# Kernel tuning notes

Measured on AMD Instinct MI355X. Metric: run time of the kernel, lower is better.

The kernel has to match this reference:

```python
import jax, jax.numpy as jnp
import numpy as np

B, S, D, H, W = 8, 2048, 128, 8, 64
INT_HEADS = 8          # hardcoded in SpatioTemporalLayer1
EPS_COS = 1e-8
EPS_LN = 1e-5


def _mha(q_in, k_in, v_in, in_w, in_b, out_w, out_b, nh, mask=None):
    # q_in/k_in/v_in: (batch, len, d); torch nn.MultiheadAttention math (eval, no dropout)
    b, lq, d = q_in.shape
    hd = d // nh
    q = (q_in @ in_w[:d].T + in_b[:d]).reshape(b, lq, nh, hd)
    k = (k_in @ in_w[d:2 * d].T + in_b[d:2 * d]).reshape(b, k_in.shape[1], nh, hd)
    v = (v_in @ in_w[2 * d:].T + in_b[2 * d:]).reshape(b, v_in.shape[1], nh, hd)
    scores = jnp.einsum('bihd,bjhd->bhij', q, k) / jnp.sqrt(jnp.asarray(hd, q_in.dtype))
    if mask is not None:
        scores = scores + mask
    attn = jax.nn.softmax(scores, axis=-1)
    out = jnp.einsum('bhij,bjhd->bihd', attn, v).reshape(b, lq, d)
    return out @ out_w.T + out_b


def _layernorm(x, g, b):
    mu = x.mean(-1, keepdims=True)
    var = ((x - mu) ** 2).mean(-1, keepdims=True)
    return (x - mu) * jax.lax.rsqrt(var + EPS_LN) * g + b


def _cos_normalize(e):
    n = jnp.maximum(jnp.linalg.norm(e, axis=-1, keepdims=True), EPS_COS)
    return e / n


def _forward(x, spatial_info, temporal_info,
             lw_in_w, lw_in_b, lw_out_w, lw_out_b,
             spat_w, spat_b, temp_w, temp_b,
             int_in_w, int_in_b, int_out_w, int_out_b,
             ffn_w1, ffn_b1, ffn_w2, ffn_b2,
             ln1_g, ln1_b, ln2_g, ln2_b):
    b, s, d = x.shape
    # --- local window attention (S % W == 0 here, so no padding path) ---
    nw = s // W
    xw = x.reshape(b * nw, W, d)
    causal = jnp.triu(jnp.full((W, W), -jnp.inf, x.dtype), k=1)
    attn = _mha(xw, xw, xw, lw_in_w, lw_in_b, lw_out_w, lw_out_b, H, causal).reshape(b, s, d)
    x = _layernorm(attn + x, ln1_g, ln1_b)
    # --- FFN (torch nn.GELU default = exact erf) ---
    h = jax.nn.gelu(x @ ffn_w1.T + ffn_b1, approximate=False)
    x = _layernorm(h @ ffn_w2.T + ffn_b2 + x, ln2_g, ln2_b)
    # --- spatio-temporal interaction ---
    se = spatial_info @ spat_w.T + spat_b
    te = temporal_info @ temp_w.T + temp_b
    sn = _cos_normalize(se)
    tn = _cos_normalize(te)
    ss = jnp.einsum('bid,bjd->bij', sn, sn)   # (B,S,S) spatial cosine sim
    ts = jnp.einsum('bid,bjd->bij', tn, tn)   # (B,S,S) temporal cosine sim
    # interaction MHA is batch_first=False: it treats (B,S,D) as (len=B, batch=S, d).
    # Equivalent batch-first call on swapped axes (faithful to the torch source).
    inter = jnp.swapaxes(
        _mha(jnp.swapaxes(se, 0, 1), jnp.swapaxes(te, 0, 1), jnp.swapaxes(te, 0, 1),
             int_in_w, int_in_b, int_out_w, int_out_b, INT_HEADS), 0, 1)
    # similarity[b,i,j,d] = ss[b,i,j]*ts[b,i,j]*inter[b,i,d]; mean over j factorizes:
    sim = (ss * ts).mean(axis=2)              # (B,S)
    return x + sim[..., None] * inter


def setup_inputs() -> dict:
    key = jax.random.key(0)
    ks = jax.random.split(key, 24)
    sc = 0.02
    inp = {
        'x': jax.random.normal(ks[0], (B, S, D), jnp.float32),
        'spatial_info': jax.random.normal(ks[1], (B, S, D), jnp.float32),
        'temporal_info': jax.random.normal(ks[2], (B, S, D), jnp.float32),
        'lw_in_w': jax.random.normal(ks[3], (3 * D, D), jnp.float32) * sc,
        'lw_in_b': jnp.zeros((3 * D,), jnp.float32),
        'lw_out_w': jax.random.normal(ks[4], (D, D), jnp.float32) * sc,
        'lw_out_b': jnp.zeros((D,), jnp.float32),
        'spat_w': jax.random.normal(ks[5], (D, D), jnp.float32) * sc,
        'spat_b': jnp.zeros((D,), jnp.float32),
        'temp_w': jax.random.normal(ks[6], (D, D), jnp.float32) * sc,
        'temp_b': jnp.zeros((D,), jnp.float32),
        'int_in_w': jax.random.normal(ks[7], (3 * D, D), jnp.float32) * sc,
        'int_in_b': jnp.zeros((3 * D,), jnp.float32),
        'int_out_w': jax.random.normal(ks[8], (D, D), jnp.float32) * sc,
        'int_out_b': jnp.zeros((D,), jnp.float32),
        'ffn_w1': jax.random.normal(ks[9], (4 * D, D), jnp.float32) * sc,
        'ffn_b1': jnp.zeros((4 * D,), jnp.float32),
        'ffn_w2': jax.random.normal(ks[10], (D, 4 * D), jnp.float32) * sc,
        'ffn_b2': jnp.zeros((D,), jnp.float32),
        'ln1_g': jnp.ones((D,), jnp.float32),
        'ln1_b': jnp.zeros((D,), jnp.float32),
        'ln2_g': jnp.ones((D,), jnp.float32),
        'ln2_b': jnp.zeros((D,), jnp.float32),
    }
    return inp


def reference(x, spatial_info, temporal_info,
              lw_in_w, lw_in_b, lw_out_w, lw_out_b,
              spat_w, spat_b, temp_w, temp_b,
              int_in_w, int_in_b, int_out_w, int_out_b,
              ffn_w1, ffn_b1, ffn_w2, ffn_b2,
              ln1_g, ln1_b, ln2_g, ln2_b):
    return _forward(x, spatial_info, temporal_info,
                    lw_in_w, lw_in_b, lw_out_w, lw_out_b,
                    spat_w, spat_b, temp_w, temp_b,
                    int_in_w, int_in_b, int_out_w, int_out_b,
                    ffn_w1, ffn_b1, ffn_w2, ffn_b2,
                    ln1_g, ln1_b, ln2_g, ln2_b)
```

## Files before the change

kernel.cpp:

```cpp
#include <hip/hip_runtime.h>
#include <math.h>

#define BB 8
#define SS 2048
#define NTOK (BB * SS)
#define ATB_SPLIT 16

using bf16x8 = __attribute__((ext_vector_type(8))) short;
using f32x4  = __attribute__((ext_vector_type(4))) float;

__device__ __forceinline__ float gelu_exact(float v) {
    return 0.5f * v * (1.0f + erff(v * 0.70710678118654752f));
}
__device__ __forceinline__ unsigned short f2b(float f) {
    unsigned int u = __float_as_uint(f);
    u += 0x7FFFu + ((u >> 16) & 1u);
    return (unsigned short)(u >> 16);
}
__device__ __forceinline__ float b2f(unsigned short u) {
    return __uint_as_float((unsigned int)u << 16);
}
__device__ __forceinline__ bf16x8 ldg_f32_b8(const float* p) {
    float4 f0 = *(const float4*)p, f1 = *(const float4*)(p + 4);
    union { ushort4 u[2]; bf16x8 v; } r;
    r.u[0] = (ushort4){f2b(f0.x), f2b(f0.y), f2b(f0.z), f2b(f0.w)};
    r.u[1] = (ushort4){f2b(f1.x), f2b(f1.y), f2b(f1.z), f2b(f1.w)};
    return r.v;
}

__global__ __launch_bounds__(256) void win_block(
    const float* __restrict__ x,
    const unsigned short* __restrict__ Wqkv,
    const float* __restrict__ b_in,
    const unsigned short* __restrict__ Wout,
    const float* __restrict__ b_out,
    const float* __restrict__ lng, const float* __restrict__ lnb,
    float* __restrict__ x1, unsigned short* __restrict__ x1b)
{
    __shared__ unsigned short Qs[64 * 136];
    __shared__ unsigned short KVs[64 * 256];
    __shared__ float red[2][64][2];
    const int tid = threadIdx.x, m0 = blockIdx.x * 64;
    const int wv = tid >> 6, lane = tid & 63, ln = lane & 15, q = lane >> 4;
    const int wm = (wv >> 1) * 32, wn = (wv & 1) * 64;

    bf16x8 afr[4][2];
    #pragma unroll
    for (int kf = 0; kf < 4; ++kf)
        #pragma unroll
        for (int fm = 0; fm < 2; ++fm)
            afr[kf][fm] = ldg_f32_b8(x + (size_t)(m0 + wm + fm * 16 + ln) * 128 + kf * 32 + q * 8);

    #pragma unroll
    for (int p = 0; p < 3; ++p) {
        f32x4 acc[2][4] = {};
        #pragma unroll
        for (int kf = 0; kf < 4; ++kf) {
            bf16x8 b[4];
            #pragma unroll
            for (int fn = 0; fn < 4; ++fn)
                b[fn] = *(const bf16x8*)&Wqkv[(size_t)(p * 128 + wn + fn * 16 + ln) * 128 + kf * 32 + q * 8];
            #pragma unroll
            for (int fm = 0; fm < 2; ++fm)
                #pragma unroll
                for (int fn = 0; fn < 4; ++fn)
                    acc[fm][fn] = __builtin_amdgcn_mfma_f32_16x16x32_bf16(afr[kf][fm], b[fn], acc[fm][fn], 0, 0, 0);
        }
        #pragma unroll
        for (int fm = 0; fm < 2; ++fm)
            #pragma unroll
            for (int r = 0; r < 4; ++r) {
                int rl = wm + fm * 16 + q * 4 + r;
                #pragma unroll
                for (int fn = 0; fn < 4; ++fn) {
                    int col = wn + fn * 16 + ln;
                    unsigned short v = f2b(acc[fm][fn][r] + b_in[p * 128 + col]);
                    if (p == 0) Qs[rl * 136 + col] = v;
                    else        KVs[rl * 256 + (p - 1) * 128 + col] = v;
                }
            }
    }
    __syncthreads();

    {
        const int l = tid & 63, hp = tid >> 6;
        #pragma unroll
        for (int hh = 0; hh < 2; ++hh) {
            const int h = hp + hh * 4;
            float qr[16];
            {
                uint4 q0 = *(const uint4*)&Qs[l * 136 + h * 16];
                uint4 q1 = *(const uint4*)&Qs[l * 136 + h * 16 + 8];
                const unsigned short* p0 = (const unsigned short*)&q0;
                const unsigned short* p1 = (const unsigned short*)&q1;
                #pragma unroll
                for (int c = 0; c < 8; ++c) { qr[c] = b2f(p0[c]); qr[8 + c] = b2f(p1[c]); }
            }
            float m = -1e30f, ssum = 0.0f, o[16] = {};
            for (int j = 0; j <= l; ++j) {
                uint4 k0 = *(const uint4*)&KVs[j * 256 + h * 16];
                uint4 k1 = *(const uint4*)&KVs[j * 256 + h * 16 + 8];
                const unsigned short* kp0 = (const unsigned short*)&k0;
                const unsigned short* kp1 = (const unsigned short*)&k1;
                float s = 0.0f;
                #pragma unroll
                for (int c = 0; c < 8; ++c) {
                    s = fmaf(qr[c], b2f(kp0[c]), s);
                    s = fmaf(qr[8 + c], b2f(kp1[c]), s);
                }
                s *= 0.25f;
                float mnew = fmaxf(m, s);
                float corr = expf(m - mnew);
                float pp = expf(s - mnew);
                ssum = ssum * corr + pp;
                uint4 v0 = *(const uint4*)&KVs[j * 256 + 128 + h * 16];
                uint4 v1 = *(const uint4*)&KVs[j * 256 + 128 + h * 16 + 8];
                const unsigned short* vp0 = (const unsigned short*)&v0;
                const unsigned short* vp1 = (const unsigned short*)&v1;
                #pragma unroll
                for (int c = 0; c < 8; ++c) {
                    o[c]     = o[c]     * corr + pp * b2f(vp0[c]);
                    o[8 + c] = o[8 + c] * corr + pp * b2f(vp1[c]);
                }
                m = mnew;
            }
            float inv = 1.0f / ssum;
            ushort4 w0, w1, w2, w3;
            w0 = (ushort4){f2b(o[0]*inv),  f2b(o[1]*inv),  f2b(o[2]*inv),  f2b(o[3]*inv)};
            w1 = (ushort4){f2b(o[4]*inv),  f2b(o[5]*inv),  f2b(o[6]*inv),  f2b(o[7]*inv)};
            w2 = (ushort4){f2b(o[8]*inv),  f2b(o[9]*inv),  f2b(o[10]*inv), f2b(o[11]*inv)};
            w3 = (ushort4){f2b(o[12]*inv), f2b(o[13]*inv), f2b(o[14]*inv), f2b(o[15]*inv)};
            *(ushort4*)&Qs[l * 136 + h * 16]      = w0;
            *(ushort4*)&Qs[l * 136 + h * 16 + 4]  = w1;
            *(ushort4*)&Qs[l * 136 + h * 16 + 8]  = w2;
            *(ushort4*)&Qs[l * 136 + h * 16 + 12] = w3;
        }
    }
    __syncthreads();

    f32x4 acc[2][4] = {};
    #pragma unroll
    for (int kf = 0; kf < 4; ++kf) {
        bf16x8 a[2], b[4];
        #pragma unroll
        for (int fm = 0; fm < 2; ++fm)
            a[fm] = *(const bf16x8*)&Qs[(wm + fm * 16 + ln) * 136 + kf * 32 + q * 8];
        #pragma unroll
        for (int fn = 0; fn < 4; ++fn)
            b[fn] = *(const bf16x8*)&Wout[(size_t)(wn + fn * 16 + ln) * 128 + kf * 32 + q * 8];
        #pragma unroll
        for (int fm = 0; fm < 2; ++fm)
            #pragma unroll
            for (int fn = 0; fn < 4; ++fn)
                acc[fm][fn] = __builtin_amdgcn_mfma_f32_16x16x32_bf16(a[fm], b[fn], acc[fm][fn], 0, 0, 0);
    }
    #pragma unroll
    for (int fm = 0; fm < 2; ++fm)
        #pragma unroll
        for (int r = 0; r < 4; ++r) {
            int rl = wm + fm * 16 + q * 4 + r;
            int row = m0 + rl;
            float s1 = 0.0f, s2 = 0.0f;
            #pragma unroll
            for (int fn = 0; fn < 4; ++fn) {
                int col = wn + fn * 16 + ln;
                float vv = acc[fm][fn][r] + b_out[col] + x[(size_t)row * 128 + col];
                acc[fm][fn][r] = vv;
                s1 += vv; s2 += vv * vv;
            }
            #pragma unroll
            for (int off = 1; off < 16; off <<= 1) {
                s1 += __shfl_xor(s1, off, 64);
                s2 += __shfl_xor(s2, off, 64);
            }
            if (ln == 0) { red[0][rl][wv & 1] = s1; red[1][rl][wv & 1] = s2; }
        }
    __syncthreads();
    #pragma unroll
    for (int fm = 0; fm < 2; ++fm)
        #pragma unroll
        for (int r = 0; r < 4; ++r) {
            int rl = wm + fm * 16 + q * 4 + r;
            int row = m0 + rl;
            float mu = (red[0][rl][0] + red[0][rl][1]) * (1.0f / 128.0f);
            float var = (red[1][rl][0] + red[1][rl][1]) * (1.0f / 128.0f) - mu * mu;
            float rs = rsqrtf(var + 1e-5f);
            #pragma unroll
            for (int fn = 0; fn < 4; ++fn) {
                int col = wn + fn * 16 + ln;
                float o = (acc[fm][fn][r] - mu) * rs * lng[col] + lnb[col];
                x1[(size_t)row * 128 + col] = o;
                x1b[(size_t)row * 128 + col] = f2b(o);
            }
        }
}

__global__ __launch_bounds__(256) void inter_block(
    const unsigned short* __restrict__ seb, const unsigned short* __restrict__ teb,
    const unsigned short* __restrict__ Wint,
    const float* __restrict__ b_int,
    const unsigned short* __restrict__ Wio,
    const float* __restrict__ b_io,
    const float* __restrict__ sim, const float* __restrict__ x2,
    float* __restrict__ out)
{
    __shared__ unsigned short Qs[64 * 136];
    __shared__ unsigned short KVs[64 * 256];
    const int tid = threadIdx.x, s0 = blockIdx.x * 8;
    const int wv = tid >> 6, lane = tid & 63, ln = lane & 15, q = lane >> 4;
    const int wm = (wv >> 1) * 32, wn = (wv & 1) * 64;

    bf16x8 afr[4][2];
    #pragma unroll
    for (int kf = 0; kf < 4; ++kf)
        #pragma unroll
        for (int fm = 0; fm < 2; ++fm) {
            int rl = wm + fm * 16 + ln;
            size_t g = (size_t)(rl >> 3) * 2048 + s0 + (rl & 7);
            afr[kf][fm] = *(const bf16x8*)&seb[g * 128 + kf * 32 + q * 8];
        }

    #pragma unroll
    for (int p = 0; p < 3; ++p) {
        if (p == 1) {
            #pragma unroll
            for (int kf = 0; kf < 4; ++kf)
                #pragma unroll
                for (int fm = 0; fm < 2; ++fm) {
                    int rl = wm + fm * 16 + ln;
                    size_t g = (size_t)(rl >> 3) * 2048 + s0 + (rl & 7);
                    afr[kf][fm] = *(const bf16x8*)&teb[g * 128 + kf * 32 + q * 8];
                }
        }
        f32x4 acc[2][4] = {};
        #pragma unroll
        for (int kf = 0; kf < 4; ++kf) {
            bf16x8 b[4];
            #pragma unroll
            for (int fn = 0; fn < 4; ++fn)
                b[fn] = *(const bf16x8*)&Wint[(size_t)(p * 128 + wn + fn * 16 + ln) * 128 + kf * 32 + q * 8];
            #pragma unroll
            for (int fm = 0; fm < 2; ++fm)
                #pragma unroll
                for (int fn = 0; fn < 4; ++fn)
                    acc[fm][fn] = __builtin_amdgcn_mfma_f32_16x16x32_bf16(afr[kf][fm], b[fn], acc[fm][fn], 0, 0, 0);
        }
        #pragma unroll
        for (int fm = 0; fm < 2; ++fm)
            #pragma unroll
            for (int r = 0; r < 4; ++r) {
                int rl = wm + fm * 16 + q * 4 + r;
                #pragma unroll
                for (int fn = 0; fn < 4; ++fn) {
                    int col = wn + fn * 16 + ln;
                    unsigned short v = f2b(acc[fm][fn][r] + b_int[p * 128 + col]);
                    if (p == 0) Qs[rl * 136 + col] = v;
                    else        KVs[rl * 256 + (p - 1) * 128 + col] = v;
                }
            }
        __syncthreads();
    }

    #pragma unroll
    for (int tt = 0; tt < 2; ++tt) {
        int task = tid + tt * 256;
        int ss = task >> 6, h = (task >> 3) & 7, i = task & 7;
        int rq = i * 8 + ss;
        float qr[16];
        {
            uint4 q0 = *(const uint4*)&Qs[rq * 136 + h * 16];
            uint4 q1 = *(const uint4*)&Qs[rq * 136 + h * 16 + 8];
            const unsigned short* p0 = (const unsigned short*)&q0;
            const unsigned short* p1 = (const unsigned short*)&q1;
            #pragma unroll
            for (int c = 0; c < 8; ++c) { qr[c] = b2f(p0[c]); qr[8 + c] = b2f(p1[c]); }
        }
        float sc[8];
        #pragma unroll
        for (int j = 0; j < 8; ++j) {
            uint4 k0 = *(const uint4*)&KVs[(j * 8 + ss) * 256 + h * 16];
            uint4 k1 = *(const uint4*)&KVs[(j * 8 + ss) * 256 + h * 16 + 8];
            const unsigned short* kp0 = (const unsigned short*)&k0;
            const unsigned short* kp1 = (const unsigned short*)&k1;
            float s = 0.0f;
            #pragma unroll
            for (int c = 0; c < 8; ++c) {
                s = fmaf(qr[c], b2f(kp0[c]), s);
                s = fmaf(qr[8 + c], b2f(kp1[c]), s);
            }
            sc[j] = s * 0.25f;
        }
        float mx = -1e30f;
        #pragma unroll
        for (int j = 0; j < 8; ++j) mx = fmaxf(mx, sc[j]);
        float pe[8], se = 0.0f;
        #pragma unroll
        for (int j = 0; j < 8; ++j) { pe[j] = expf(sc[j] - mx); se += pe[j]; }
        float inv = 1.0f / se;
        float o[16] = {};
        #pragma unroll
        for (int j = 0; j < 8; ++j) {
            uint4 v0 = *(const uint4*)&KVs[(j * 8 + ss) * 256 + 128 + h * 16];
            uint4 v1 = *(const uint4*)&KVs[(j * 8 + ss) * 256 + 128 + h * 16 + 8];
            const unsigned short* vp0 = (const unsigned short*)&v0;
            const unsigned short* vp1 = (const unsigned short*)&v1;
            #pragma unroll
            for (int c = 0; c < 8; ++c) {
                o[c]     += pe[j] * b2f(vp0[c]);
                o[8 + c] += pe[j] * b2f(vp1[c]);
            }
        }
        ushort4 w0 = (ushort4){f2b(o[0]*inv),  f2b(o[1]*inv),  f2b(o[2]*inv),  f2b(o[3]*inv)};
        ushort4 w1 = (ushort4){f2b(o[4]*inv),  f2b(o[5]*inv),  f2b(o[6]*inv),  f2b(o[7]*inv)};
        ushort4 w2 = (ushort4){f2b(o[8]*inv),  f2b(o[9]*inv),  f2b(o[10]*inv), f2b(o[11]*inv)};
        ushort4 w3 = (ushort4){f2b(o[12]*inv), f2b(o[13]*inv), f2b(o[14]*inv), f2b(o[15]*inv)};
        *(ushort4*)&Qs[rq * 136 + h * 16]      = w0;
        *(ushort4*)&Qs[rq * 136 + h * 16 + 4]  = w1;
        *(ushort4*)&Qs[rq * 136 + h * 16 + 8]  = w2;
        *(ushort4*)&Qs[rq * 136 + h * 16 + 12] = w3;
    }
    __syncthreads();

    f32x4 acc[2][4] = {};
    #pragma unroll
    for (int kf = 0; kf < 4; ++kf) {
        bf16x8 a[2], b[4];
        #pragma unroll
        for (int fm = 0; fm < 2; ++fm)
            a[fm] = *(const bf16x8*)&Qs[(wm + fm * 16 + ln) * 136 + kf * 32 + q * 8];
        #pragma unroll
        for (int fn = 0; fn < 4; ++fn)
            b[fn] = *(const bf16x8*)&Wio[(size_t)(wn + fn * 16 + ln) * 128 + kf * 32 + q * 8];
        #pragma unroll
        for (int fm = 0; fm < 2; ++fm)
            #pragma unroll
            for (int fn = 0; fn < 4; ++fn)
                acc[fm][fn] = __builtin_amdgcn_mfma_f32_16x16x32_bf16(a[fm], b[fn], acc[fm][fn], 0, 0, 0);
    }
    #pragma unroll
    for (int fm = 0; fm < 2; ++fm)
        #pragma unroll
        for (int r = 0; r < 4; ++r) {
            int rl = wm + fm * 16 + q * 4 + r;
            size_t g = (size_t)(rl >> 3) * 2048 + s0 + (rl & 7);
            float sc = sim[g];
            #pragma unroll
            for (int fn = 0; fn < 4; ++fn) {
                int col = wn + fn * 16 + ln;
                out[g * 128 + col] = (acc[fm][fn][r] + b_io[col]) * sc + x2[g * 128 + col];
            }
        }
}

__global__ __launch_bounds__(256) void ffn_fused(
    const unsigned short* __restrict__ x1b, const float* __restrict__ x1,
    const unsigned short* __restrict__ w1, const unsigned short* __restrict__ w2,
    const float* __restrict__ b1, const float* __restrict__ b2,
    const float* __restrict__ lng, const float* __restrict__ lnb,
    float* __restrict__ x2)
{
    __shared__ unsigned short Xs[64 * 136];
    __shared__ unsigned short Hs[64 * 72];
    __shared__ float red[2][64][2];
    const int tid = threadIdx.x, t0 = blockIdx.x * 64;
    const int wv = tid >> 6, lane = tid & 63, ln = lane & 15, q = lane >> 4;
    const int wm = (wv >> 1) * 32;
    const int wn1 = (wv & 1) * 32, wn2 = (wv & 1) * 64;

    const uint4* X4 = (const uint4*)(x1b + (size_t)t0 * 128);
    #pragma unroll
    for (int t = 0; t < 4; ++t) {
        int idx = tid + t * 256;
        int r = idx >> 4, c = idx & 15;
        *(uint4*)&Xs[r * 136 + c * 8] = X4[r * 16 + c];
    }
    __syncthreads();

    bf16x8 xfr[4][2];
    #pragma unroll
    for (int kf = 0; kf < 4; ++kf)
        #pragma unroll
        for (int fm = 0; fm < 2; ++fm)
            xfr[kf][fm] = *(const bf16x8*)&Xs[(wm + fm * 16 + ln) * 136 + kf * 32 + q * 8];

    f32x4 acc2[2][4] = {};
    for (int ch = 0; ch < 8; ++ch) {
        const int hc0 = ch * 64;
        f32x4 acc1[2][2] = {};
        #pragma unroll
        for (int kf = 0; kf < 4; ++kf) {
            bf16x8 b[2];
            #pragma unroll
            for (int fn = 0; fn < 2; ++fn)
                b[fn] = *(const bf16x8*)&w1[(size_t)(hc0 + wn1 + fn * 16 + ln) * 128 + kf * 32 + q * 8];
            #pragma unroll
            for (int fm = 0; fm < 2; ++fm)
                #pragma unroll
                for (int fn = 0; fn < 2; ++fn)
                    acc1[fm][fn] = __builtin_amdgcn_mfma_f32_16x16x32_bf16(xfr[kf][fm], b[fn], acc1[fm][fn], 0, 0, 0);
        }
        #pragma unroll
        for (int fm = 0; fm < 2; ++fm)
            #pragma unroll
            for (int fn = 0; fn < 2; ++fn)
                #pragma unroll
                for (int r = 0; r < 4; ++r) {
                    int rl = wm + fm * 16 + q * 4 + r;
                    int col = wn1 + fn * 16 + ln;
                    Hs[rl * 72 + col] = f2b(gelu_exact(acc1[fm][fn][r] + b1[hc0 + col]));
                }
        __syncthreads();
        #pragma unroll
        for (int kf = 0; kf < 2; ++kf) {
            bf16x8 a[2], b[4];
            #pragma unroll
            for (int fm = 0; fm < 2; ++fm)
                a[fm] = *(const bf16x8*)&Hs[(wm + fm * 16 + ln) * 72 + kf * 32 + q * 8];
            #pragma unroll
            for (int fn = 0; fn < 4; ++fn)
                b[fn] = *(const bf16x8*)&w2[(size_t)(wn2 + fn * 16 + ln) * 512 + hc0 + kf * 32 + q * 8];
            #pragma unroll
            for (int fm = 0; fm < 2; ++fm)
                #pragma unroll
                for (int fn = 0; fn < 4; ++fn)
                    acc2[fm][fn] = __builtin_amdgcn_mfma_f32_16x16x32_bf16(a[fm], b[fn], acc2[fm][fn], 0, 0, 0);
        }
        __syncthreads();
    }
    #pragma unroll
    for (int fm = 0; fm < 2; ++fm)
        #pragma unroll
        for (int r = 0; r < 4; ++r) {
            int rl = wm + fm * 16 + q * 4 + r;
            int row = t0 + rl;
            float s1 = 0.0f, s2 = 0.0f;
            #pragma unroll
            for (int fn = 0; fn < 4; ++fn) {
                int col = wn2 + fn * 16 + ln;
                float vv = acc2[fm][fn][r] + b2[col] + x1[(size_t)row * 128 + col];
                acc2[fm][fn][r] = vv;
                s1 += vv; s2 += vv * vv;
            }
            #pragma unroll
            for (int off = 1; off < 16; off <<= 1) {
                s1 += __shfl_xor(s1, off, 64);
                s2 += __shfl_xor(s2, off, 64);
            }
            if (ln == 0) { red[0][rl][wv & 1] = s1; red[1][rl][wv & 1] = s2; }
        }
    __syncthreads();
    #pragma unroll
    for (int fm = 0; fm < 2; ++fm)
        #pragma unroll
        for (int r = 0; r < 4; ++r) {
            int rl = wm + fm * 16 + q * 4 + r;
            int row = t0 + rl;
            float mu = (red[0][rl][0] + red[0][rl][1]) * (1.0f / 128.0f);
            float var = (red[1][rl][0] + red[1][rl][1]) * (1.0f / 128.0f) - mu * mu;
            float rs = rsqrtf(var + 1e-5f);
            #pragma unroll
            for (int fn = 0; fn < 4; ++fn) {
                int col = wn2 + fn * 16 + ln;
                x2[(size_t)row * 128 + col] = (acc2[fm][fn][r] - mu) * rs * lng[col] + lnb[col];
            }
        }
}

__global__ __launch_bounds__(256) void stproj_kernel(
    const float* __restrict__ sp, const float* __restrict__ tp,
    const unsigned short* __restrict__ Wsp, const unsigned short* __restrict__ Wtp,
    const float* __restrict__ bsp, const float* __restrict__ btp,
    float* __restrict__ sn, float* __restrict__ tn,
    unsigned short* __restrict__ snb,
    unsigned short* __restrict__ seb, unsigned short* __restrict__ teb)
{
    __shared__ float red[64][2];
    const int tid = threadIdx.x, m0 = blockIdx.x * 64, y = blockIdx.y;
    const float* Af = y ? tp : sp;
    const unsigned short* W = y ? Wtp : Wsp;
    const float* bias = y ? btp : bsp;
    float* nrm = y ? tn : sn;
    unsigned short* nb = y ? nullptr : snb;
    unsigned short* raw = y ? teb : seb;
    const int wv = tid >> 6, lane = tid & 63, ln = lane & 15, q = lane >> 4;
    const int wm = (wv >> 1) * 32, wn = (wv & 1) * 64;

    f32x4 acc[2][4] = {};
    #pragma unroll
    for (int kf = 0; kf < 4; ++kf) {
        bf16x8 a[2], b[4];
        #pragma unroll
        for (int fm = 0; fm < 2; ++fm)
            a[fm] = ldg_f32_b8(Af + (size_t)(m0 + wm + fm * 16 + ln) * 128 + kf * 32 + q * 8);
        #pragma unroll
        for (int fn = 0; fn < 4; ++fn)
            b[fn] = *(const bf16x8*)&W[(size_t)(wn + fn * 16 + ln) * 128 + kf * 32 + q * 8];
        #pragma unroll
        for (int fm = 0; fm < 2; ++fm)
            #pragma unroll
            for (int fn = 0; fn < 4; ++fn)
                acc[fm][fn] = __builtin_amdgcn_mfma_f32_16x16x32_bf16(a[fm], b[fn], acc[fm][fn], 0, 0, 0);
    }
    #pragma unroll
    for (int fm = 0; fm < 2; ++fm)
        #pragma unroll
        for (int r = 0; r < 4; ++r) {
            int rl = wm + fm * 16 + q * 4 + r;
            float s2 = 0.0f;
            #pragma unroll
            for (int fn = 0; fn < 4; ++fn) {
                int col = wn + fn * 16 + ln;
                float vv = acc[fm][fn][r] + bias[col];
                acc[fm][fn][r] = vv;
                s2 += vv * vv;
            }
            #pragma unroll
            for (int off = 1; off < 16; off <<= 1) s2 += __shfl_xor(s2, off, 64);
            if (ln == 0) red[rl][wv & 1] = s2;
        }
    __syncthreads();
    #pragma unroll
    for (int fm = 0; fm < 2; ++fm)
        #pragma unroll
        for (int r = 0; r < 4; ++r) {
            int rl = wm + fm * 16 + q * 4 + r;
            int row = m0 + rl;
            float inv = 1.0f / fmaxf(sqrtf(red[rl][0] + red[rl][1]), 1e-8f);
            #pragma unroll
            for (int fn = 0; fn < 4; ++fn) {
                int col = wn + fn * 16 + ln;
                float vv = acc[fm][fn][r];
                float nv = vv * inv;
                nrm[(size_t)row * 128 + col] = nv;
                if (nb != nullptr) nb[(size_t)row * 128 + col] = f2b(nv);
                raw[(size_t)row * 128 + col] = f2b(vv);
            }
        }
}

__global__ __launch_bounds__(256) void simgemm_kernel(
    const unsigned short* __restrict__ snb, const float* __restrict__ tn,
    const unsigned short* __restrict__ Mtb, float* __restrict__ sim)
{
    __shared__ float red[64][2];
    const int tid = threadIdx.x, m0 = blockIdx.x * 64, b = m0 >> 11;
    const int wv = tid >> 6, lane = tid & 63, ln = lane & 15, q = lane >> 4;
    const int wm = (wv >> 1) * 32, wn = (wv & 1) * 64;

    f32x4 acc[2][4] = {};
    #pragma unroll
    for (int kf = 0; kf < 4; ++kf) {
        bf16x8 a[2], bb[4];
        #pragma unroll
        for (int fm = 0; fm < 2; ++fm)
            a[fm] = *(const bf16x8*)&snb[(size_t)(m0 + wm + fm * 16 + ln) * 128 + kf * 32 + q * 8];
        #pragma unroll
        for (int fn = 0; fn < 4; ++fn)
            bb[fn] = *(const bf16x8*)&Mtb[(size_t)b * 16384 + (size_t)(wn + fn * 16 + ln) * 128 + kf * 32 + q * 8];
        #pragma unroll
        for (int fm = 0; fm < 2; ++fm)
            #pragma unroll
            for (int fn = 0; fn < 4; ++fn)
                acc[fm][fn] = __builtin_amdgcn_mfma_f32_16x16x32_bf16(a[fm], bb[fn], acc[fm][fn], 0, 0, 0);
    }
    #pragma unroll
    for (int fm = 0; fm < 2; ++fm)
        #pragma unroll
        for (int r = 0; r < 4; ++r) {
            int rl = wm + fm * 16 + q * 4 + r;
            int row = m0 + rl;
            float s = 0.0f;
            #pragma unroll
            for (int fn = 0; fn < 4; ++fn) {
                int col = wn + fn * 16 + ln;
                s += acc[fm][fn][r] * tn[(size_t)row * 128 + col];
            }
            #pragma unroll
            for (int off = 1; off < 16; off <<= 1) s += __shfl_xor(s, off, 64);
            if (ln == 0) red[rl][wv & 1] = s;
        }
    __syncthreads();
    if (tid < 64) sim[m0 + tid] = (red[tid][0] + red[tid][1]) * (1.0f / (float)SS);
}

__global__ __launch_bounds__(256) void convertW_kernel(
    const float* __restrict__ w0, const float* __restrict__ w1,
    const float* __restrict__ w2, const float* __restrict__ w3,
    const float* __restrict__ w4, const float* __restrict__ w5,
    const float* __restrict__ w6, const float* __restrict__ w7,
    unsigned short* __restrict__ dst)
{
    int i = blockIdx.x * 256 + threadIdx.x;
    const float* s; int base;
    if      (i < 49152)  { s = w0; base = 0; }
    else if (i < 65536)  { s = w1; base = 49152; }
    else if (i < 131072) { s = w2; base = 65536; }
    else if (i < 196608) { s = w3; base = 131072; }
    else if (i < 212992) { s = w4; base = 196608; }
    else if (i < 229376) { s = w5; base = 212992; }
    else if (i < 278528) { s = w6; base = 229376; }
    else                 { s = w7; base = 278528; }
    dst[i] = f2b(s[i - base]);
}

__global__ __launch_bounds__(256) void atb_split_kernel(
    const float* __restrict__ sn, const float* __restrict__ tn,
    float* __restrict__ part)
{
    const int b = blockIdx.z / ATB_SPLIT;
    const int chunk = blockIdx.z % ATB_SPLIT;
    const int d0 = blockIdx.x * 64, e0 = blockIdx.y * 64;
    __shared__ float Ss[32][68];
    __shared__ float Ts[32][68];
    const int tid = threadIdx.x;
    const int tx = tid % 16, ty = tid / 16;
    const float* sb = sn + (size_t)b * SS * 128;
    const float* tb = tn + (size_t)b * SS * 128;
    const int jbase = chunk * (SS / ATB_SPLIT);
    float acc[4][4] = {};
    for (int j0 = jbase; j0 < jbase + SS / ATB_SPLIT; j0 += 32) {
        #pragma unroll
        for (int it = 0; it < 2; ++it) {
            int idx = tid + it * 256;
            int r = idx / 16, c4 = (idx % 16) * 4;
            *(float4*)&Ss[r][c4] = *(const float4*)&sb[(size_t)(j0 + r) * 128 + d0 + c4];
            *(float4*)&Ts[r][c4] = *(const float4*)&tb[(size_t)(j0 + r) * 128 + e0 + c4];
        }
        __syncthreads();
        #pragma unroll
        for (int kk = 0; kk < 32; ++kk) {
            float4 af = *(const float4*)&Ss[kk][ty * 4];
            float4 wf = *(const float4*)&Ts[kk][tx * 4];
            float a[4] = {af.x, af.y, af.z, af.w};
            float w[4] = {wf.x, wf.y, wf.z, wf.w};
            #pragma unroll
            for (int i = 0; i < 4; ++i)
                #pragma unroll
                for (int j = 0; j < 4; ++j)
                    acc[i][j] = fmaf(a[i], w[j], acc[i][j]);
        }
        __syncthreads();
    }
    float* pp = part + (size_t)(b * ATB_SPLIT + chunk) * 16384;
    #pragma unroll
    for (int i = 0; i < 4; ++i) {
        float4 ov = {acc[i][0], acc[i][1], acc[i][2], acc[i][3]};
        *(float4*)&pp[(size_t)(d0 + ty * 4 + i) * 128 + e0 + tx * 4] = ov;
    }
}

__global__ __launch_bounds__(256) void atb_reduce_kernel(
    const float* __restrict__ part, unsigned short* __restrict__ Mtb)
{
    int i = blockIdx.x * 256 + threadIdx.x;
    int b = i >> 14, rem = i & 16383;
    int e = rem >> 7, d = rem & 127;
    const float* pp = part + (size_t)b * ATB_SPLIT * 16384 + (size_t)d * 128 + e;
    float s = 0.0f;
    #pragma unroll
    for (int c = 0; c < ATB_SPLIT; ++c) s += pp[(size_t)c * 16384];
    Mtb[i] = f2b(s);
}

extern "C" void kernel_launch(void* const* d_in, const int* in_sizes, int n_in,
                              void* d_out, int out_size, void* d_ws, size_t ws_size,
                              hipStream_t stream)
{
    const float* x        = (const float*)d_in[0];
    const float* spatial  = (const float*)d_in[1];
    const float* temporal = (const float*)d_in[2];
    const float* lw_in_b  = (const float*)d_in[4];
    const float* lw_out_b = (const float*)d_in[6];
    const float* spat_b   = (const float*)d_in[8];
    const float* temp_b   = (const float*)d_in[10];
    const float* int_in_b = (const float*)d_in[12];
    const float* int_out_b= (const float*)d_in[14];
    const float* ffn_b1   = (const float*)d_in[16];
    const float* ffn_b2   = (const float*)d_in[18];
    const float* ln1_g    = (const float*)d_in[19];
    const float* ln1_b    = (const float*)d_in[20];
    const float* ln2_g    = (const float*)d_in[21];
    const float* ln2_b    = (const float*)d_in[22];
    float* out = (float*)d_out;

    char* base = (char*)d_ws;
    float*          x1   = (float*)(base + 0);
    unsigned short* x1b  = (unsigned short*)(base + 8388608);
    float*          x2   = (float*)(base + 12582912);
    float*          sn   = (float*)(base + 20971520);
    float*          tn   = (float*)(base + 29360128);
    unsigned short* seb  = (unsigned short*)(base + 37748736);
    unsigned short* teb  = (unsigned short*)(base + 41943040);
    unsigned short* snb  = (unsigned short*)(base + 46137344);
    unsigned short* Mtb  = (unsigned short*)(base + 50331648);
    float*          simb = (float*)(base + 50593792);
    unsigned short* Wb   = (unsigned short*)(base + 50659328);
    float*          part = x1;

    unsigned short* Wb_lwin  = Wb + 0;
    unsigned short* Wb_lwout = Wb + 49152;
    unsigned short* Wb_ffn1  = Wb + 65536;
    unsigned short* Wb_ffn2  = Wb + 131072;
    unsigned short* Wb_spat  = Wb + 196608;
    unsigned short* Wb_temp  = Wb + 212992;
    unsigned short* Wb_intin = Wb + 229376;
    unsigned short* Wb_intout= Wb + 278528;

    convertW_kernel<<<1152, 256, 0, stream>>>(
        (const float*)d_in[3], (const float*)d_in[5], (const float*)d_in[15],
        (const float*)d_in[17], (const float*)d_in[7], (const float*)d_in[9],
        (const float*)d_in[11], (const float*)d_in[13], Wb);
    win_block<<<256, 256, 0, stream>>>(
        x, Wb_lwin, lw_in_b, Wb_lwout, lw_out_b, ln1_g, ln1_b, x1, x1b);
    ffn_fused<<<256, 256, 0, stream>>>(
        x1b, x1, Wb_ffn1, Wb_ffn2, ffn_b1, ffn_b2, ln2_g, ln2_b, x2);
    stproj_kernel<<<dim3(256, 2), 256, 0, stream>>>(
        spatial, temporal, Wb_spat, Wb_temp, spat_b, temp_b,
        sn, tn, snb, seb, teb);
    atb_split_kernel<<<dim3(2, 2, 8 * ATB_SPLIT), 256, 0, stream>>>(sn, tn, part);
    atb_reduce_kernel<<<512, 256, 0, stream>>>(part, Mtb);
    simgemm_kernel<<<256, 256, 0, stream>>>(snb, tn, Mtb, simb);
    inter_block<<<256, 256, 0, stream>>>(
        seb, teb, Wb_intin, int_in_b, Wb_intout, int_out_b, simb, x2, out);
}
```

Baseline: 259.9 us.

## Compute causal window attention with MFMA tiles instead of scalar online softmax

The per-thread scalar online-softmax loop over keys in the window-attention block is replaced by bf16 MFMA matrix products. QK^T is computed per head with zero-padded K=32 fragments, then the causal mask and a row softmax use 16-lane shuffles, and P·V is done with MFMA against a transposed V layout in shared memory. The aim is to remove the long serial dependent FMA/exp chain and the imbalance across threads from causal lengths. The trade-offs are extra shared memory for the per-wave P buffers and transposed V, and rounding the probabilities to bf16. A second kernel also swaps expf for the faster __expf.

```diff
diff --git a/kernel.cpp b/kernel.cpp
--- a/kernel.cpp
+++ b/kernel.cpp
@@ -38,7 +38,9 @@
     float* __restrict__ x1, unsigned short* __restrict__ x1b)
 {
     __shared__ unsigned short Qs[64 * 136];
-    __shared__ unsigned short KVs[64 * 256];
+    __shared__ unsigned short Ks[64 * 136];
+    __shared__ unsigned short Vt[128 * 72];
+    __shared__ unsigned short Pb[4][32 * 72];
     __shared__ float red[2][64][2];
     const int tid = threadIdx.x, m0 = blockIdx.x * 64;
     const int wv = tid >> 6, lane = tid & 63, ln = lane & 15, q = lane >> 4;
@@ -75,65 +77,86 @@
                 for (int fn = 0; fn < 4; ++fn) {
                     int col = wn + fn * 16 + ln;
                     unsigned short v = f2b(acc[fm][fn][r] + b_in[p * 128 + col]);
-                    if (p == 0) Qs[rl * 136 + col] = v;
-                    else        KVs[rl * 256 + (p - 1) * 128 + col] = v;
+                    if (p == 0)      Qs[rl * 136 + col] = v;
+                    else if (p == 1) Ks[rl * 136 + col] = v;
+                    else             Vt[col * 72 + rl] = v;
                 }
             }
     }
     __syncthreads();
 
     {
-        const int l = tid & 63, hp = tid >> 6;
-        #pragma unroll
-        for (int hh = 0; hh < 2; ++hh) {
-            const int h = hp + hh * 4;
-            float qr[16];
-            {
-                uint4 q0 = *(const uint4*)&Qs[l * 136 + h * 16];
-                uint4 q1 = *(const uint4*)&Qs[l * 136 + h * 16 + 8];
-                const unsigned short* p0 = (const unsigned short*)&q0;
-                const unsigned short* p1 = (const unsigned short*)&q1;
-                #pragma unroll
-                for (int c = 0; c < 8; ++c) { qr[c] = b2f(p0[c]); qr[8 + c] = b2f(p1[c]); }
-            }
-            float m = -1e30f, ssum = 0.0f, o[16] = {};
-            for (int j = 0; j <= l; ++j) {
-                uint4 k0 = *(const uint4*)&KVs[j * 256 + h * 16];
-                uint4 k1 = *(const uint4*)&KVs[j * 256 + h * 16 + 8];
-                const unsigned short* kp0 = (const unsigned short*)&k0;
-                const unsigned short* kp1 = (const unsigned short*)&k1;
-                float s = 0.0f;
-                #pragma unroll
-                for (int c = 0; c < 8; ++c) {
-                    s = fmaf(qr[c], b2f(kp0[c]), s);
-                    s = fmaf(qr[8 + c], b2f(kp1[c]), s);
+        const int mh = wv >> 1, hq = wv & 1;
+        unsigned short* P = &Pb[wv][0];
+        #pragma unroll
+        for (int hh = 0; hh < 4; ++hh) {
+            const int h = hq * 4 + hh;
+            f32x4 sacc[2][4] = {};
+            bf16x8 az[2] = {}, bz[4] = {};
+            if (q < 2) {
+                #pragma unroll
+                for (int fm = 0; fm < 2; ++fm)
+                    az[fm] = *(const bf16x8*)&Qs[(mh * 32 + fm * 16 + ln) * 136 + h * 16 + q * 8];
+                #pragma unroll
+                for (int fn = 0; fn < 4; ++fn)
+                    bz[fn] = *(const bf16x8*)&Ks[(fn * 16 + ln) * 136 + h * 16 + q * 8];
+            }
+            #pragma unroll
+            for (int fm = 0; fm < 2; ++fm)
+                #pragma unroll
+                for (int fn = 0; fn < 4; ++fn)
+                    sacc[fm][fn] = __builtin_amdgcn_mfma_f32_16x16x32_bf16(az[fm], bz[fn], sacc[fm][fn], 0, 0, 0);
+            float invr[2][4];
+            #pragma unroll
+            for (int fm = 0; fm < 2; ++fm)
+                #pragma unroll
+                for (int r = 0; r < 4; ++r) {
+                    int gi = mh * 32 + fm * 16 + q * 4 + r;
+                    float mx = -1e30f;
+                    #pragma unroll
+                    for (int fn = 0; fn < 4; ++fn) {
+                        int j = fn * 16 + ln;
+                        float s = sacc[fm][fn][r] * 0.25f;
+                        if (j > gi) s = -1e30f;
+                        sacc[fm][fn][r] = s;
+                        mx = fmaxf(mx, s);
+                    }
+                    #pragma unroll
+                    for (int off = 1; off < 16; off <<= 1)
+                        mx = fmaxf(mx, __shfl_xor(mx, off, 64));
+                    float sum = 0.0f;
+                    #pragma unroll
+                    for (int fn = 0; fn < 4; ++fn) {
+                        float p_ = __expf(sacc[fm][fn][r] - mx);
+                        sacc[fm][fn][r] = p_;
+                        sum += p_;
+                    }
+                    #pragma unroll
+                    for (int off = 1; off < 16; off <<= 1)
+                        sum += __shfl_xor(sum, off, 64);
+                    invr[fm][r] = 1.0f / sum;
+                    #pragma unroll
+                    for (int fn = 0; fn < 4; ++fn)
+                        P[(fm * 16 + q * 4 + r) * 72 + fn * 16 + ln] = f2b(sacc[fm][fn][r]);
                 }
-                s *= 0.25f;
-                float mnew = fmaxf(m, s);
-                float corr = expf(m - mnew);
-                float pp = expf(s - mnew);
-                ssum = ssum * corr + pp;
-                uint4 v0 = *(const uint4*)&KVs[j * 256 + 128 + h * 16];
-                uint4 v1 = *(const uint4*)&KVs[j * 256 + 128 + h * 16 + 8];
-                const unsigned short* vp0 = (const unsigned short*)&v0;
-                const unsigned short* vp1 = (const unsigned short*)&v1;
-                #pragma unroll
-                for (int c = 0; c < 8; ++c) {
-                    o[c]     = o[c]     * corr + pp * b2f(vp0[c]);
-                    o[8 + c] = o[8 + c] * corr + pp * b2f(vp1[c]);
-                }
-                m = mnew;
-            }
-            float inv = 1.0f / ssum;
-            ushort4 w0, w1, w2, w3;
-            w0 = (ushort4){f2b(o[0]*inv),  f2b(o[1]*inv),  f2b(o[2]*inv),  f2b(o[3]*inv)};
-            w1 = (ushort4){f2b(o[4]*inv),  f2b(o[5]*inv),  f2b(o[6]*inv),  f2b(o[7]*inv)};
-            w2 = (ushort4){f2b(o[8]*inv),  f2b(o[9]*inv),  f2b(o[10]*inv), f2b(o[11]*inv)};
-            w3 = (ushort4){f2b(o[12]*inv), f2b(o[13]*inv), f2b(o[14]*inv), f2b(o[15]*inv)};
-            *(ushort4*)&Qs[l * 136 + h * 16]      = w0;
-            *(ushort4*)&Qs[l * 136 + h * 16 + 4]  = w1;
-            *(ushort4*)&Qs[l * 136 + h * 16 + 8]  = w2;
-            *(ushort4*)&Qs[l * 136 + h * 16 + 12] = w3;
+            f32x4 oacc[2] = {};
+            #pragma unroll
+            for (int kf2 = 0; kf2 < 2; ++kf2) {
+                bf16x8 pa[2], vb;
+                #pragma unroll
+                for (int fm = 0; fm < 2; ++fm)
+                    pa[fm] = *(const bf16x8*)&P[(fm * 16 + ln) * 72 + kf2 * 32 + q * 8];
+                vb = *(const bf16x8*)&Vt[(h * 16 + ln) * 72 + kf2 * 32 + q * 8];
+                #pragma unroll
+                for (int fm = 0; fm < 2; ++fm)
+                    oacc[fm] = __builtin_amdgcn_mfma_f32_16x16x32_bf16(pa[fm], vb, oacc[fm], 0, 0, 0);
+            }
+            #pragma unroll
+            for (int fm = 0; fm < 2; ++fm)
+                #pragma unroll
+                for (int r = 0; r < 4; ++r)
+                    Qs[(mh * 32 + fm * 16 + q * 4 + r) * 136 + h * 16 + ln] =
+                        f2b(oacc[fm][r] * invr[fm][r]);
         }
     }
     __syncthreads();
@@ -295,7 +318,7 @@
         for (int j = 0; j < 8; ++j) mx = fmaxf(mx, sc[j]);
         float pe[8], se = 0.0f;
         #pragma unroll
-        for (int j = 0; j < 8; ++j) { pe[j] = expf(sc[j] - mx); se += pe[j]; }
+        for (int j = 0; j < 8; ++j) { pe[j] = __expf(sc[j] - mx); se += pe[j]; }
         float inv = 1.0f / se;
         float o[16] = {};
         #pragma unroll
```

Result: faster. 241.4 us (-7.1%).
